# Kernel optimization log

Measured on AMD Instinct MI355X. Metric: run time of the kernel, lower is better.

The kernel has to match this reference:

```python
import jax, jax.numpy as jnp
import numpy as np


def setup_inputs() -> dict:
    key = jax.random.key(0)
    k1, k2, k3 = jax.random.split(key, 3)
    N, Q, K, E = 8, 2048, 2048, 512
    query = jax.random.normal(k1, (N, Q, E), dtype=jnp.float32)
    keys = jax.random.normal(k2, (N, K, E), dtype=jnp.float32)
    values = jax.random.normal(k3, (N, K, E), dtype=jnp.float32)
    return {"query": query, "keys": keys, "values": values}


def reference(query, keys, values):
    # energy: [N, Q, K] -- note: NO 1/sqrt(d) scaling, matching the original
    energy = jnp.einsum('nqe,nke->nqk', query, keys)
    attention = jax.nn.softmax(energy, axis=-1)
    out = jnp.einsum('nqk,nke->nqe', attention, values)
    return out
```

## Files before the change

### kernel.cpp

```cpp
#include <hip/hip_runtime.h>
#include <stdint.h>


typedef __attribute__((ext_vector_type(8))) _Float16 half8;
typedef __attribute__((ext_vector_type(2))) _Float16 half2;
typedef __attribute__((ext_vector_type(4))) float    floatx4;

#define NBATCH 8
#define SEQ    2048
#define EDIM   512
static constexpr size_t NE = (size_t)NBATCH * SEQ * EDIM;

__device__ __forceinline__ void block_sync_lds() {
  asm volatile("s_waitcnt lgkmcnt(0)\n\ts_barrier" ::: "memory");
}

__device__ __forceinline__ half8 cvt8(float4 a, float4 b) {
  half8 h;
  h[0] = (_Float16)a.x; h[1] = (_Float16)a.y; h[2] = (_Float16)a.z; h[3] = (_Float16)a.w;
  h[4] = (_Float16)b.x; h[5] = (_Float16)b.y; h[6] = (_Float16)b.z; h[7] = (_Float16)b.w;
  return h;
}


__global__ void make_frags(const float* __restrict__ k, const float* __restrict__ v,
                           _Float16* __restrict__ kf, _Float16* __restrict__ vf) {
  __shared__ float lds[32][260];
  const int tid = threadIdx.x;
  const int seg = blockIdx.x >> 9;
  const int b   = blockIdx.x & 511;
  const int n = b >> 6, kt = b & 63;
  const float* src = (seg == 0 ? k : v) + ((size_t)n * SEQ + kt * 32) * EDIM;

  if (seg == 0) {
    _Float16* dst = kf + ((size_t)(n * 128 + kt * 2) * 16) * 512;
#pragma unroll
    for (int eh = 0; eh < 2; eh++) {
      if (eh) __syncthreads();
#pragma unroll
      for (int i = 0; i < 8; i++) {
        int c = i * 256 + tid;
        int row = c >> 6, col4 = c & 63;
        float4 x = *reinterpret_cast<const float4*>(src + (size_t)row * EDIM + eh * 256 + col4 * 4);
        *reinterpret_cast<float4*>(&lds[row][col4 * 4]) = x;
      }
      __syncthreads();
#pragma unroll
      for (int i = 0; i < 4; i++) {
        int fl = i * 256 + tid;
        int lane = fl & 63, idx = fl >> 6;
        int est_l = idx & 7, rt_l = idx >> 3;
        int m15 = lane & 15, q4 = lane >> 4;
        const float* p = &lds[rt_l * 16 + m15][est_l * 32 + q4 * 8];
        float4 a = *reinterpret_cast<const float4*>(p);
        float4 bb = *reinterpret_cast<const float4*>(p + 4);
        *reinterpret_cast<half8*>(dst + ((size_t)(rt_l * 16 + eh * 8 + est_l)) * 512 + lane * 8) =
            cvt8(a, bb);
      }
    }
  } else {
    _Float16* dst = vf + ((size_t)(n * 64 + kt) * 32) * 512;
#pragma unroll
    for (int eh = 0; eh < 2; eh++) {
      if (eh) __syncthreads();
#pragma unroll
      for (int i = 0; i < 8; i++) {
        int c = i * 256 + tid;
        int row = c >> 6, col4 = c & 63;
        float4 x = *reinterpret_cast<const float4*>(src + (size_t)row * EDIM + eh * 256 + col4 * 4);
        *reinterpret_cast<float4*>(&lds[row][col4 * 4]) = x;
      }
      __syncthreads();
#pragma unroll
      for (int i = 0; i < 4; i++) {
        int fl = i * 256 + tid;
        int etl = fl >> 6, ln = fl & 63;
        int m15 = ln & 15, q4 = ln >> 4;
        int e_local = etl * 16 + m15;
        half8 h;
#pragma unroll
        for (int j = 0; j < 8; j++) h[j] = (_Float16)lds[q4 * 8 + j][e_local];
        *reinterpret_cast<half8*>(dst + ((size_t)eh * 1024 + fl) * 8) = h;
      }
    }
  }
}

__launch_bounds__(512, 4)
__global__ void attn_fused(const float* __restrict__ q, const _Float16* __restrict__ kf,
                           const _Float16* __restrict__ vf, float* __restrict__ out) {
  __shared__ float    s_part[4][32][36];
  __shared__ _Float16 p_lds[32][40];
  __shared__ float    m_lds[32], l_lds[32], a_lds[32];

  const int tid  = threadIdx.x;
  const int lane = tid & 63, w = tid >> 6;
  const int m15  = lane & 15, q4 = lane >> 4;
  const int n    = blockIdx.x & 7, qt = blockIdx.x >> 3;
  const int ks   = w & 1, es = w >> 1;

  if (tid < 32) { m_lds[tid] = -3.0e38f; l_lds[tid] = 0.0f; }

  half8 qfr[2][4];
  {
    const float* qb = q + ((size_t)n * SEQ + qt * 32 + m15) * EDIM + es * 128 + q4 * 8;
#pragma unroll
    for (int s = 0; s < 2; s++)
#pragma unroll
      for (int i = 0; i < 4; i++) {
        const float* src = qb + (size_t)s * 16 * EDIM + i * 32;
        float4 a = *reinterpret_cast<const float4*>(src);
        float4 b = *reinterpret_cast<const float4*>(src + 4);
        qfr[s][i] = cvt8(a, b);
      }
  }

  floatx4 oacc[2][4];
#pragma unroll
  for (int s = 0; s < 2; s++)
#pragma unroll
    for (int j = 0; j < 4; j++) oacc[s][j] = (floatx4){0.f, 0.f, 0.f, 0.f};

  uint32_t koff = ((uint32_t)(n * 128 + ks) * 16 + es * 4) * 512 + (uint32_t)lane * 8;
  uint32_t voff = ((uint32_t)(n * 64) * 32 + w * 4) * 512 + (uint32_t)lane * 8;

  half8 kcur[4];
#pragma unroll
  for (int i = 0; i < 4; i++)
    kcur[i] = *reinterpret_cast<const half8*>(kf + koff + (uint32_t)i * 512);
  koff += 16384;

  block_sync_lds();

  for (int t = 0; t < 64; t++) {
    floatx4 sacc[2];
    sacc[0] = (floatx4){0.f, 0.f, 0.f, 0.f};
    sacc[1] = (floatx4){0.f, 0.f, 0.f, 0.f};
    __builtin_amdgcn_s_setprio(1);
#pragma unroll
    for (int i = 0; i < 4; i++) {
      sacc[0] = __builtin_amdgcn_mfma_f32_16x16x32_f16(qfr[0][i], kcur[i], sacc[0], 0, 0, 0);
      sacc[1] = __builtin_amdgcn_mfma_f32_16x16x32_f16(qfr[1][i], kcur[i], sacc[1], 0, 0, 0);
    }
    __builtin_amdgcn_s_setprio(0);

    half8 knxt[4];
#pragma unroll
    for (int i = 0; i < 4; i++)
      knxt[i] = *reinterpret_cast<const half8*>(kf + koff + (uint32_t)i * 512);
    koff += 16384;

    half8 vfr[4];
#pragma unroll
    for (int j = 0; j < 4; j++)
      vfr[j] = *reinterpret_cast<const half8*>(vf + voff + (uint32_t)j * 512);
    voff += 16384;

#pragma unroll
    for (int s = 0; s < 2; s++)
#pragma unroll
      for (int r = 0; r < 4; r++)
        s_part[es][s * 16 + q4 * 4 + r][ks * 16 + m15] = sacc[s][r];
    block_sync_lds();

    {
      const int r = tid >> 4, sub = tid & 15, c = sub * 2;
      float svx = s_part[0][r][c],     svy = s_part[0][r][c + 1];
#pragma unroll
      for (int pl = 1; pl < 4; pl++) { svx += s_part[pl][r][c]; svy += s_part[pl][r][c + 1]; }
      float mx = fmaxf(svx, svy);
#pragma unroll
      for (int o = 1; o < 16; o <<= 1) mx = fmaxf(mx, __shfl_xor(mx, o));
      const float mo = m_lds[r];
      const float mn = fmaxf(mo, mx);
      const float px = __expf(svx - mn), py = __expf(svy - mn);
      float rs = px + py;
#pragma unroll
      for (int o = 1; o < 16; o <<= 1) rs += __shfl_xor(rs, o);
      if (sub == 0) {
        const float al = __expf(mo - mn);
        a_lds[r] = al; m_lds[r] = mn; l_lds[r] = l_lds[r] * al + rs;
      }
      half2 ph; ph[0] = (_Float16)px; ph[1] = (_Float16)py;
      *reinterpret_cast<half2*>(&p_lds[r][c]) = ph;
    }
    block_sync_lds();

    half8 pfr[2];
    pfr[0] = *reinterpret_cast<const half8*>(&p_lds[m15][q4 * 8]);
    pfr[1] = *reinterpret_cast<const half8*>(&p_lds[16 + m15][q4 * 8]);
    {
      floatx4 al0 = *reinterpret_cast<floatx4*>(&a_lds[q4 * 4]);
      floatx4 al1 = *reinterpret_cast<floatx4*>(&a_lds[16 + q4 * 4]);
#pragma unroll
      for (int j = 0; j < 4; j++) { oacc[0][j] *= al0; oacc[1][j] *= al1; }
    }
    __builtin_amdgcn_s_setprio(1);
#pragma unroll
    for (int j = 0; j < 4; j++) {
      oacc[0][j] = __builtin_amdgcn_mfma_f32_16x16x32_f16(pfr[0], vfr[j], oacc[0][j], 0, 0, 0);
      oacc[1][j] = __builtin_amdgcn_mfma_f32_16x16x32_f16(pfr[1], vfr[j], oacc[1][j], 0, 0, 0);
    }
    __builtin_amdgcn_s_setprio(0);

#pragma unroll
    for (int i = 0; i < 4; i++) kcur[i] = knxt[i];
  }

  const int q0 = qt * 32;
#pragma unroll
  for (int s = 0; s < 2; s++) {
    floatx4 lv = *reinterpret_cast<floatx4*>(&l_lds[s * 16 + q4 * 4]);
#pragma unroll
    for (int j = 0; j < 4; j++) {
      const int col = (w * 4 + j) * 16 + m15;
#pragma unroll
      for (int r = 0; r < 4; r++) {
        const int row = s * 16 + q4 * 4 + r;
        out[((size_t)n * SEQ + q0 + row) * EDIM + col] = oacc[s][j][r] / lv[r];
      }
    }
  }
}

__global__ void attn_fallback(const float* __restrict__ q, const float* __restrict__ k,
                              const float* __restrict__ v, float* __restrict__ out) {
  __shared__ float qrow[EDIM];
  __shared__ float sc[SEQ];
  __shared__ float red[16];
  const int tid = threadIdx.x;
  const int n = blockIdx.x >> 11, qi = blockIdx.x & 2047;
  const int wv = tid >> 6, ln = tid & 63;
  const float* qp = q + ((size_t)n * SEQ + qi) * EDIM;
  for (int e = tid; e < EDIM; e += 256) qrow[e] = qp[e];
  __syncthreads();
  for (int kk = wv; kk < SEQ; kk += 4) {
    const float* kp = k + ((size_t)n * SEQ + kk) * EDIM;
    float s = 0.f;
    for (int e = ln; e < EDIM; e += 64) s = fmaf(qrow[e], kp[e], s);
    for (int o = 32; o > 0; o >>= 1) s += __shfl_down(s, o);
    if (ln == 0) sc[kk] = s;
  }
  __syncthreads();
  float mx = -3.0e38f;
  for (int kk = tid; kk < SEQ; kk += 256) mx = fmaxf(mx, sc[kk]);
  for (int o = 32; o > 0; o >>= 1) mx = fmaxf(mx, __shfl_down(mx, o));
  if (ln == 0) red[wv] = mx;
  __syncthreads();
  if (tid == 0) {
    float m2 = red[0];
    for (int i = 1; i < 4; i++) m2 = fmaxf(m2, red[i]);
    red[8] = m2;
  }
  __syncthreads();
  const float m = red[8];
  float ls = 0.f;
  for (int kk = tid; kk < SEQ; kk += 256) { float p = __expf(sc[kk] - m); sc[kk] = p; ls += p; }
  for (int o = 32; o > 0; o >>= 1) ls += __shfl_down(ls, o);
  if (ln == 0) red[wv] = ls;
  __syncthreads();
  if (tid == 0) { red[9] = red[0] + red[1] + red[2] + red[3]; }
  __syncthreads();
  const float linv = 1.f / red[9];
  for (int e = tid; e < EDIM; e += 256) {
    float acc = 0.f;
    const float* vp = v + ((size_t)n * SEQ) * EDIM + e;
    for (int kk = 0; kk < SEQ; kk++) acc = fmaf(sc[kk], vp[(size_t)kk * EDIM], acc);
    out[((size_t)n * SEQ + qi) * EDIM + e] = acc * linv;
  }
}

extern "C" void kernel_launch(void* const* d_in, const int* in_sizes, int n_in,
                              void* d_out, int out_size, void* d_ws, size_t ws_size,
                              hipStream_t stream) {
  const float* q = (const float*)d_in[0];
  const float* k = (const float*)d_in[1];
  const float* v = (const float*)d_in[2];
  float* out = (float*)d_out;
  const size_t need = 2 * NE * sizeof(_Float16);
  if (ws_size >= need) {
    _Float16* kf = (_Float16*)d_ws;
    _Float16* vf = kf + NE;
    make_frags<<<1024, 256, 0, stream>>>(k, v, kf, vf);
    attn_fused<<<512, 512, 0, stream>>>(q, kf, vf, out);
  } else {
    attn_fallback<<<16384, 256, 0, stream>>>(q, k, v, out);
  }
}
```

Measured before the change: 234.9 us.

## Double key tile per iteration to 64 keys and drop K register prefetch

Each loop iteration now handles 64 keys instead of 32, so the loop runs 32 times instead of 64. This halves the number of barriers, LDS partial-sum exchanges and online-softmax rescale steps. Shared arrays are widened with new padding to hold the larger tile. The K register double-buffering is removed, and K is now loaded at the top of each iteration, so those loads are exposed latency unless the compiler or occupancy hides them. Register use also rises with the larger fragments.

```diff
diff --git a/kernel.cpp b/kernel.cpp
--- a/kernel.cpp
+++ b/kernel.cpp
@@ -3,7 +3,7 @@
 
 
 typedef __attribute__((ext_vector_type(8))) _Float16 half8;
-typedef __attribute__((ext_vector_type(2))) _Float16 half2;
+typedef __attribute__((ext_vector_type(4))) _Float16 half4;
 typedef __attribute__((ext_vector_type(4))) float    floatx4;
 
 #define NBATCH 8
@@ -89,8 +89,8 @@
 __launch_bounds__(512, 4)
 __global__ void attn_fused(const float* __restrict__ q, const _Float16* __restrict__ kf,
                            const _Float16* __restrict__ vf, float* __restrict__ out) {
-  __shared__ float    s_part[4][32][36];
-  __shared__ _Float16 p_lds[32][40];
+  __shared__ float    s_part[4][32][69];
+  __shared__ _Float16 p_lds[32][72];
   __shared__ float    m_lds[32], l_lds[32], a_lds[32];
 
   const int tid  = threadIdx.x;
@@ -121,74 +121,88 @@
 #pragma unroll
     for (int j = 0; j < 4; j++) oacc[s][j] = (floatx4){0.f, 0.f, 0.f, 0.f};
 
-  uint32_t koff = ((uint32_t)(n * 128 + ks) * 16 + es * 4) * 512 + (uint32_t)lane * 8;
+  uint32_t koff = ((uint32_t)(n * 128 + ks * 2) * 16 + es * 4) * 512 + (uint32_t)lane * 8;
   uint32_t voff = ((uint32_t)(n * 64) * 32 + w * 4) * 512 + (uint32_t)lane * 8;
 
-  half8 kcur[4];
-#pragma unroll
-  for (int i = 0; i < 4; i++)
-    kcur[i] = *reinterpret_cast<const half8*>(kf + koff + (uint32_t)i * 512);
-  koff += 16384;
-
   block_sync_lds();
 
-  for (int t = 0; t < 64; t++) {
-    floatx4 sacc[2];
-    sacc[0] = (floatx4){0.f, 0.f, 0.f, 0.f};
-    sacc[1] = (floatx4){0.f, 0.f, 0.f, 0.f};
+  for (int t = 0; t < 32; t++) {
+    half8 kfr[2][4];
+#pragma unroll
+    for (int kb = 0; kb < 2; kb++)
+#pragma unroll
+      for (int i = 0; i < 4; i++)
+        kfr[kb][i] = *reinterpret_cast<const half8*>(kf + koff + (uint32_t)(kb * 16 + i) * 512);
+    koff += 32768;
+
+    floatx4 sacc[2][2];
+#pragma unroll
+    for (int s = 0; s < 2; s++)
+#pragma unroll
+      for (int kb = 0; kb < 2; kb++) sacc[s][kb] = (floatx4){0.f, 0.f, 0.f, 0.f};
     __builtin_amdgcn_s_setprio(1);
 #pragma unroll
-    for (int i = 0; i < 4; i++) {
-      sacc[0] = __builtin_amdgcn_mfma_f32_16x16x32_f16(qfr[0][i], kcur[i], sacc[0], 0, 0, 0);
-      sacc[1] = __builtin_amdgcn_mfma_f32_16x16x32_f16(qfr[1][i], kcur[i], sacc[1], 0, 0, 0);
-    }
+    for (int i = 0; i < 4; i++)
+#pragma unroll
+      for (int kb = 0; kb < 2; kb++) {
+        sacc[0][kb] = __builtin_amdgcn_mfma_f32_16x16x32_f16(qfr[0][i], kfr[kb][i], sacc[0][kb], 0, 0, 0);
+        sacc[1][kb] = __builtin_amdgcn_mfma_f32_16x16x32_f16(qfr[1][i], kfr[kb][i], sacc[1][kb], 0, 0, 0);
+      }
     __builtin_amdgcn_s_setprio(0);
 
-    half8 knxt[4];
-#pragma unroll
-    for (int i = 0; i < 4; i++)
-      knxt[i] = *reinterpret_cast<const half8*>(kf + koff + (uint32_t)i * 512);
-    koff += 16384;
-
-    half8 vfr[4];
-#pragma unroll
-    for (int j = 0; j < 4; j++)
-      vfr[j] = *reinterpret_cast<const half8*>(vf + voff + (uint32_t)j * 512);
-    voff += 16384;
+    half8 vfr[2][4];
+#pragma unroll
+    for (int kc = 0; kc < 2; kc++)
+#pragma unroll
+      for (int j = 0; j < 4; j++)
+        vfr[kc][j] = *reinterpret_cast<const half8*>(vf + voff + (uint32_t)(kc * 32 + j) * 512);
+    voff += 32768;
 
 #pragma unroll
     for (int s = 0; s < 2; s++)
 #pragma unroll
-      for (int r = 0; r < 4; r++)
-        s_part[es][s * 16 + q4 * 4 + r][ks * 16 + m15] = sacc[s][r];
+      for (int kb = 0; kb < 2; kb++)
+#pragma unroll
+        for (int r = 0; r < 4; r++)
+          s_part[es][s * 16 + q4 * 4 + r][(ks * 2 + kb) * 16 + m15] = sacc[s][kb][r];
     block_sync_lds();
 
     {
-      const int r = tid >> 4, sub = tid & 15, c = sub * 2;
-      float svx = s_part[0][r][c],     svy = s_part[0][r][c + 1];
-#pragma unroll
-      for (int pl = 1; pl < 4; pl++) { svx += s_part[pl][r][c]; svy += s_part[pl][r][c + 1]; }
-      float mx = fmaxf(svx, svy);
+      const int r = tid >> 4, sub = tid & 15, c = sub * 4;
+      float sv[4];
+#pragma unroll
+      for (int x = 0; x < 4; x++) {
+        float acc = s_part[0][r][c + x];
+#pragma unroll
+        for (int pl = 1; pl < 4; pl++) acc += s_part[pl][r][c + x];
+        sv[x] = acc;
+      }
+      float mx = fmaxf(fmaxf(sv[0], sv[1]), fmaxf(sv[2], sv[3]));
 #pragma unroll
       for (int o = 1; o < 16; o <<= 1) mx = fmaxf(mx, __shfl_xor(mx, o));
       const float mo = m_lds[r];
       const float mn = fmaxf(mo, mx);
-      const float px = __expf(svx - mn), py = __expf(svy - mn);
-      float rs = px + py;
+      float p0 = __expf(sv[0] - mn), p1 = __expf(sv[1] - mn);
+      float p2 = __expf(sv[2] - mn), p3 = __expf(sv[3] - mn);
+      float rs = (p0 + p1) + (p2 + p3);
 #pragma unroll
       for (int o = 1; o < 16; o <<= 1) rs += __shfl_xor(rs, o);
       if (sub == 0) {
         const float al = __expf(mo - mn);
         a_lds[r] = al; m_lds[r] = mn; l_lds[r] = l_lds[r] * al + rs;
       }
-      half2 ph; ph[0] = (_Float16)px; ph[1] = (_Float16)py;
-      *reinterpret_cast<half2*>(&p_lds[r][c]) = ph;
+      half4 ph;
+      ph[0] = (_Float16)p0; ph[1] = (_Float16)p1; ph[2] = (_Float16)p2; ph[3] = (_Float16)p3;
+      *reinterpret_cast<half4*>(&p_lds[r][c]) = ph;
     }
     block_sync_lds();
 
-    half8 pfr[2];
-    pfr[0] = *reinterpret_cast<const half8*>(&p_lds[m15][q4 * 8]);
-    pfr[1] = *reinterpret_cast<const half8*>(&p_lds[16 + m15][q4 * 8]);
+    half8 pfr[2][2];
+#pragma unroll
+    for (int s = 0; s < 2; s++)
+#pragma unroll
+      for (int kc = 0; kc < 2; kc++)
+        pfr[s][kc] = *reinterpret_cast<const half8*>(&p_lds[s * 16 + m15][kc * 32 + q4 * 8]);
     {
       floatx4 al0 = *reinterpret_cast<floatx4*>(&a_lds[q4 * 4]);
       floatx4 al1 = *reinterpret_cast<floatx4*>(&a_lds[16 + q4 * 4]);
@@ -197,14 +211,13 @@
     }
     __builtin_amdgcn_s_setprio(1);
 #pragma unroll
-    for (int j = 0; j < 4; j++) {
-      oacc[0][j] = __builtin_amdgcn_mfma_f32_16x16x32_f16(pfr[0], vfr[j], oacc[0][j], 0, 0, 0);
-      oacc[1][j] = __builtin_amdgcn_mfma_f32_16x16x32_f16(pfr[1], vfr[j], oacc[1][j], 0, 0, 0);
-    }
+    for (int j = 0; j < 4; j++)
+#pragma unroll
+      for (int kc = 0; kc < 2; kc++) {
+        oacc[0][j] = __builtin_amdgcn_mfma_f32_16x16x32_f16(pfr[0][kc], vfr[kc][j], oacc[0][j], 0, 0, 0);
+        oacc[1][j] = __builtin_amdgcn_mfma_f32_16x16x32_f16(pfr[1][kc], vfr[kc][j], oacc[1][j], 0, 0, 0);
+      }
     __builtin_amdgcn_s_setprio(0);
-
-#pragma unroll
-    for (int i = 0; i < 4; i++) kcur[i] = knxt[i];
   }
 
   const int q0 = qt * 32;
```

Result: slower. 248.4 us (+5.8%).
